# Performance work log

Measured on AMD Instinct MI355X. Metric: run time of the kernel, lower is better.

Reference implementation:

```python
import jax, jax.numpy as jnp
import numpy as np

EPS = 1e-5  # torch BatchNorm1d default

def _silu(x):
    return x * jax.nn.sigmoid(x)

def _bn(x, g, b, rm, rv, axis):
    # eval-mode batchnorm along given channel axis
    shape = [1] * x.ndim
    shape[axis] = -1
    return (x - rm.reshape(shape)) * (g.reshape(shape) / jnp.sqrt(rv.reshape(shape) + EPS)) + b.reshape(shape)

def setup_inputs() -> dict:
    key = jax.random.key(0)
    ks = jax.random.split(key, 12)
    b, n, p, d, r = 64, 256, 12, 128, 2
    x = jax.random.normal(ks[0], (b, n, p, d), dtype=jnp.float32)
    # k branch: Conv1d(p -> 1, k=1, bias=False) + BN(1)
    wk = jax.random.normal(ks[1], (p,), dtype=jnp.float32) / np.sqrt(p)
    bn_k_g = jax.random.uniform(ks[2], (1,), dtype=jnp.float32, minval=0.5, maxval=1.5)
    bn_k_b = 0.1 * jax.random.normal(ks[3], (1,), dtype=jnp.float32)
    bn_k_rm = jnp.zeros((1,), jnp.float32)
    bn_k_rv = jnp.ones((1,), jnp.float32)
    # v branch: Conv1d(d -> d, k=1, bias=False) + BN(d)
    wv = jax.random.normal(ks[4], (d, d), dtype=jnp.float32) / np.sqrt(d)
    bn_v_g = jax.random.uniform(ks[5], (d,), dtype=jnp.float32, minval=0.5, maxval=1.5)
    bn_v_b = 0.1 * jax.random.normal(ks[6], (d,), dtype=jnp.float32)
    bn_v_rm = jnp.zeros((d,), jnp.float32)
    bn_v_rv = jnp.ones((d,), jnp.float32)
    # fc_avg / fc_max: Linear(n, n//r, bias=False) -> GELU -> Linear(n//r, n, bias=False)
    w_avg1 = jax.random.normal(ks[7], (n // r, n), dtype=jnp.float32) / np.sqrt(n)
    w_avg2 = jax.random.normal(ks[8], (n, n // r), dtype=jnp.float32) / np.sqrt(n // r)
    w_max1 = jax.random.normal(ks[9], (n // r, n), dtype=jnp.float32) / np.sqrt(n)
    w_max2 = jax.random.normal(ks[10], (n, n // r), dtype=jnp.float32) / np.sqrt(n // r)
    return dict(x=x, wk=wk, bn_k_g=bn_k_g, bn_k_b=bn_k_b, bn_k_rm=bn_k_rm, bn_k_rv=bn_k_rv,
                wv=wv, bn_v_g=bn_v_g, bn_v_b=bn_v_b, bn_v_rm=bn_v_rm, bn_v_rv=bn_v_rv,
                w_avg1=w_avg1, w_avg2=w_avg2, w_max1=w_max1, w_max2=w_max2)

def _forward(x, wk, bn_k_g, bn_k_b, bn_k_rm, bn_k_rv, wv, bn_v_g, bn_v_b, bn_v_rm, bn_v_rv,
             w_avg1, w_avg2, w_max1, w_max2):
    b, n, p, d = x.shape
    xf = x.reshape(b * n, p, d)
    # squeeze-excite gates: pool over d, FC over n
    avg = jnp.mean(xf, axis=-1).reshape(b, n, p).transpose(0, 2, 1)  # [b,p,n]
    mx = jnp.max(xf, axis=-1).reshape(b, n, p).transpose(0, 2, 1)    # [b,p,n]
    gelu = lambda t: jax.nn.gelu(t, approximate=False)
    avg_g = jax.nn.sigmoid(gelu(avg @ w_avg1.T) @ w_avg2.T).transpose(0, 2, 1)  # [b,n,p]
    max_g = jax.nn.sigmoid(gelu(mx @ w_max1.T) @ w_max2.T).transpose(0, 2, 1)   # [b,n,p]
    # k: 1x1 conv over p channels -> [bn, d], BN(1ch), SiLU, softmax over d
    k_raw = jnp.einsum('bpd,p->bd', xf, wk)
    k = jax.nn.softmax(_silu(k_raw * (bn_k_g / jnp.sqrt(bn_k_rv + EPS)) - bn_k_rm * (bn_k_g / jnp.sqrt(bn_k_rv + EPS)) + bn_k_b), axis=-1)  # [bn,d]
    # v: 1x1 conv over d channels on [bn,d,p], BN(d), SiLU -> [bn,p,d]
    v_raw = jnp.einsum('bpd,ed->bpe', xf, wv)  # channel axis is last here
    v = _silu(_bn(v_raw, bn_v_g, bn_v_b, bn_v_rm, bn_v_rv, axis=2))  # [bn,p,d]
    # y = v @ k : [bn,p];  y_pool = (max+avg) @ v : [bn,d]
    y = jnp.einsum('bpd,bd->bp', v, k)
    pool = (max_g + avg_g).reshape(b * n, p)
    y_pool = jnp.einsum('bp,bpd->bd', pool, v)
    out = y_pool[:, None, :] * y[:, :, None]  # [bn,p,d]
    return out.reshape(b, n, p, d)

def reference(x, wk, bn_k_g, bn_k_b, bn_k_rm, bn_k_rv, wv, bn_v_g, bn_v_b, bn_v_rm, bn_v_rv,
              w_avg1, w_avg2, w_max1, w_max2):
    return _forward(x, wk, bn_k_g, bn_k_b, bn_k_rm, bn_k_rv, wv, bn_v_g, bn_v_b, bn_v_rm, bn_v_rv,
                    w_avg1, w_avg2, w_max1, w_max2)
```

## Files before the change

kernel.cpp:

```cpp
#include <hip/hip_runtime.h>
#include <hip/hip_bf16.h>

#define B_   64
#define N_   256
#define P_   12
#define D_   128
#define BN_  (B_*N_)
#define EPSV 1e-5f

typedef float  f32x4  __attribute__((ext_vector_type(4)));
typedef __bf16 bf16x8 __attribute__((ext_vector_type(8)));
typedef __bf16 bf16x4 __attribute__((ext_vector_type(4)));

__device__ float g_avg[768*256];
__device__ float g_mx [768*256];
__device__ float g_h1 [1536*128];
__device__ float g_pool[BN_*P_];

__device__ inline float sigm_(float x) { return 1.0f / (1.0f + __expf(-x)); }

__device__ inline float dot4_(float4 a, float4 b, float acc) {
  acc = fmaf(a.x, b.x, acc); acc = fmaf(a.y, b.y, acc);
  acc = fmaf(a.z, b.z, acc); acc = fmaf(a.w, b.w, acc);
  return acc;
}

__global__ __launch_bounds__(256) void k1_pool(const float* __restrict__ x) {
  int w = threadIdx.x >> 6, l = threadIdx.x & 63;
  int bn = blockIdx.x * 4 + w;
  const float* xp = x + (size_t)bn * (P_ * D_);
  int half = l >> 5, lane32 = l & 31;
  float s6[6], m6[6];
#pragma unroll
  for (int pp = 0; pp < 6; ++pp) {
    int p = pp * 2 + half;
    float4 v = *(const float4*)(xp + p * D_ + lane32 * 4);
    float s = (v.x + v.y) + (v.z + v.w);
    float m = fmaxf(fmaxf(v.x, v.y), fmaxf(v.z, v.w));
#pragma unroll
    for (int off = 16; off; off >>= 1) {
      s += __shfl_xor(s, off);
      m = fmaxf(m, __shfl_xor(m, off));
    }
    s6[pp] = s * (1.0f / D_);
    m6[pp] = m;
  }
  if (lane32 == 0) {
    int b = bn >> 8, n = bn & 255;
#pragma unroll
    for (int pp = 0; pp < 6; ++pp) {
      int p = pp * 2 + half;
      g_avg[(b * P_ + p) * N_ + n] = s6[pp];
      g_mx [(b * P_ + p) * N_ + n] = m6[pp];
    }
  }
}

__global__ __launch_bounds__(256) void k2_l1(const float* __restrict__ w_avg1,
                                             const float* __restrict__ w_max1) {
  __shared__ float in_t[16 * 256];
  __shared__ float w_t[64 * 68];
  int t = threadIdx.x;
  int rblk = blockIdx.x % 96, cblk = blockIdx.x / 96;
  int rr0 = rblk * 16, c0 = cblk * 64;
  bool mxb = (rr0 >= 768);
  int r768 = mxb ? rr0 - 768 : rr0;
  const float* in = (mxb ? g_mx : g_avg) + (size_t)r768 * 256;
  const float* w1 = mxb ? w_max1 : w_avg1;
#pragma unroll
  for (int i = 0; i < 4; ++i) {
    int F = t + i * 256, r = F >> 6, k4 = F & 63;
    *(float4*)(in_t + r * 256 + k4 * 4) = *(const float4*)(in + r * 256 + k4 * 4);
  }
  int c = t & 63, rq = t >> 6;
  float a0 = 0, a1 = 0, a2 = 0, a3 = 0;
  for (int kc = 0; kc < 4; ++kc) {
    __syncthreads();
#pragma unroll
    for (int i = 0; i < 4; ++i) {
      int F = t + i * 256, cr = F >> 4, k4 = F & 15;
      *(float4*)(w_t + cr * 68 + k4 * 4) =
          *(const float4*)(w1 + (size_t)(c0 + cr) * 256 + kc * 64 + k4 * 4);
    }
    __syncthreads();
#pragma unroll
    for (int k4 = 0; k4 < 16; ++k4) {
      float4 wv4 = *(float4*)(w_t + c * 68 + k4 * 4);
      a0 = dot4_(*(float4*)(in_t + (rq * 4 + 0) * 256 + kc * 64 + k4 * 4), wv4, a0);
      a1 = dot4_(*(float4*)(in_t + (rq * 4 + 1) * 256 + kc * 64 + k4 * 4), wv4, a1);
      a2 = dot4_(*(float4*)(in_t + (rq * 4 + 2) * 256 + kc * 64 + k4 * 4), wv4, a2);
      a3 = dot4_(*(float4*)(in_t + (rq * 4 + 3) * 256 + kc * 64 + k4 * 4), wv4, a3);
    }
  }
  float accs[4] = {a0, a1, a2, a3};
#pragma unroll
  for (int r = 0; r < 4; ++r) {
    float a = accs[r];
    float g = 0.5f * a * (1.0f + erff(a * 0.70710678f));
    g_h1[(size_t)(rr0 + rq * 4 + r) * 128 + c0 + c] = g;
  }
}

__global__ __launch_bounds__(256) void k2_l2(const float* __restrict__ w_avg2,
                                             const float* __restrict__ w_max2) {
  __shared__ float ina_t[16 * 128];
  __shared__ float inm_t[16 * 128];
  __shared__ float wa_t[64 * 68];
  __shared__ float wm_t[64 * 68];
  int t = threadIdx.x;
  int rblk = blockIdx.x % 48, cblk = blockIdx.x / 48;
  int rr0 = rblk * 16, n0 = cblk * 64;
#pragma unroll
  for (int i = 0; i < 2; ++i) {
    int F = t + i * 256, r = F >> 5, k4 = F & 31;
    *(float4*)(ina_t + r * 128 + k4 * 4) = *(const float4*)(g_h1 + (size_t)(rr0 + r) * 128 + k4 * 4);
    *(float4*)(inm_t + r * 128 + k4 * 4) = *(const float4*)(g_h1 + (size_t)(768 + rr0 + r) * 128 + k4 * 4);
  }
  int c = t & 63, rq = t >> 6;
  float aa0=0, aa1=0, aa2=0, aa3=0, am0=0, am1=0, am2=0, am3=0;
  for (int kc = 0; kc < 2; ++kc) {
    __syncthreads();
#pragma unroll
    for (int i = 0; i < 4; ++i) {
      int F = t + i * 256, cr = F >> 4, k4 = F & 15;
      *(float4*)(wa_t + cr * 68 + k4 * 4) =
          *(const float4*)(w_avg2 + (size_t)(n0 + cr) * 128 + kc * 64 + k4 * 4);
      *(float4*)(wm_t + cr * 68 + k4 * 4) =
          *(const float4*)(w_max2 + (size_t)(n0 + cr) * 128 + kc * 64 + k4 * 4);
    }
    __syncthreads();
#pragma unroll
    for (int k4 = 0; k4 < 16; ++k4) {
      float4 wa4 = *(float4*)(wa_t + c * 68 + k4 * 4);
      float4 wm4 = *(float4*)(wm_t + c * 68 + k4 * 4);
      float4 i0 = *(float4*)(ina_t + (rq * 4 + 0) * 128 + kc * 64 + k4 * 4);
      float4 i1 = *(float4*)(ina_t + (rq * 4 + 1) * 128 + kc * 64 + k4 * 4);
      float4 i2 = *(float4*)(ina_t + (rq * 4 + 2) * 128 + kc * 64 + k4 * 4);
      float4 i3 = *(float4*)(ina_t + (rq * 4 + 3) * 128 + kc * 64 + k4 * 4);
      aa0 = dot4_(i0, wa4, aa0); aa1 = dot4_(i1, wa4, aa1);
      aa2 = dot4_(i2, wa4, aa2); aa3 = dot4_(i3, wa4, aa3);
      float4 j0 = *(float4*)(inm_t + (rq * 4 + 0) * 128 + kc * 64 + k4 * 4);
      float4 j1 = *(float4*)(inm_t + (rq * 4 + 1) * 128 + kc * 64 + k4 * 4);
      float4 j2 = *(float4*)(inm_t + (rq * 4 + 2) * 128 + kc * 64 + k4 * 4);
      float4 j3 = *(float4*)(inm_t + (rq * 4 + 3) * 128 + kc * 64 + k4 * 4);
      am0 = dot4_(j0, wm4, am0); am1 = dot4_(j1, wm4, am1);
      am2 = dot4_(j2, wm4, am2); am3 = dot4_(j3, wm4, am3);
    }
  }
  float va[4] = {aa0, aa1, aa2, aa3};
  float vm[4] = {am0, am1, am2, am3};
#pragma unroll
  for (int r = 0; r < 4; ++r) {
    int rr = rr0 + rq * 4 + r;
    int b = rr / 12, p = rr % 12;
    float pv = sigm_(va[r]) + sigm_(vm[r]);
    g_pool[((size_t)b * 256 + (n0 + c)) * 12 + p] = pv;
  }
}

__global__ __launch_bounds__(256) void k3_main(
    const float* __restrict__ x,  const float* __restrict__ wk,
    const float* __restrict__ kg, const float* __restrict__ kb,
    const float* __restrict__ krm, const float* __restrict__ krv,
    const float* __restrict__ wv,
    const float* __restrict__ vg, const float* __restrict__ vb,
    const float* __restrict__ vrm, const float* __restrict__ vrv,
    float* __restrict__ out) {
  __shared__ __align__(16) __bf16 wv_lds[128 * 128];
  __shared__ float sv_l[128], tv_l[128];
  __shared__ float k_lds[4][128];
  __shared__ float yp_l[4][128];
  __shared__ __align__(16) float y_l[4][16];

  int t = threadIdx.x, w = t >> 6, l = t & 63;
  if (t < 128) {
    float s = vg[t] * rsqrtf(vrv[t] + EPSV);
    sv_l[t] = s;
    tv_l[t] = vb[t] - vrm[t] * s;
  }
  __syncthreads();
  {
    int e = t >> 1, dh = (t & 1) * 64;
    float s = sv_l[e];
    int swz = (e & 7) << 4;
#pragma unroll
    for (int i = 0; i < 16; ++i) {
      float4 v4 = *(const float4*)(wv + (size_t)e * 128 + dh + i * 4);
      bf16x4 h;
      h[0] = (__bf16)(v4.x * s); h[1] = (__bf16)(v4.y * s);
      h[2] = (__bf16)(v4.z * s); h[3] = (__bf16)(v4.w * s);
      int byte = (e * 256 + (dh + i * 4) * 2) ^ swz;
      *(bf16x4*)((char*)wv_lds + byte) = h;
    }
  }
  float ksc = kg[0] * rsqrtf(krv[0] + EPSV);
  float kbs = kb[0] - krm[0] * ksc;
  float wkl[P_];
#pragma unroll
  for (int p = 0; p < P_; ++p) wkl[p] = wk[p];
  __syncthreads();

  int arow = (l & 15) > 11 ? 11 : (l & 15);
  int ak = (l >> 4) * 8;
  int bcol = l & 15;
  int bko = (l >> 4) * 16;
  int p0 = (l >> 4) * 4;
  bool rows_ok = (p0 < 12);

  float tv_e[8];
#pragma unroll
  for (int nt = 0; nt < 8; ++nt) tv_e[nt] = tv_l[bcol + nt * 16];

  for (int it = 0; it < 4; ++it) {
    int bn = blockIdx.x * 16 + it * 4 + w;
    const float* xp = x + (size_t)bn * (P_ * D_);

    float pool_r[4] = {0.f, 0.f, 0.f, 0.f};
    if (rows_ok) {
      const float* pp = g_pool + (size_t)bn * 12 + p0;
#pragma unroll
      for (int r = 0; r < 4; ++r) pool_r[r] = pp[r];
    }

    bf16x8 afr[4];
#pragma unroll
    for (int ks = 0; ks < 4; ++ks) {
      const float* src = xp + arow * 128 + ks * 32 + ak;
      float4 lo = *(const float4*)(src);
      float4 hi = *(const float4*)(src + 4);
      bf16x8 a;
      a[0] = (__bf16)lo.x; a[1] = (__bf16)lo.y; a[2] = (__bf16)lo.z; a[3] = (__bf16)lo.w;
      a[4] = (__bf16)hi.x; a[5] = (__bf16)hi.y; a[6] = (__bf16)hi.z; a[7] = (__bf16)hi.w;
      afr[ks] = a;
    }

    float kr0 = 0, kr1 = 0;
#pragma unroll
    for (int p = 0; p < P_; ++p) {
      float2 xv = *(const float2*)(xp + p * 128 + 2 * l);
      kr0 = fmaf(xv.x, wkl[p], kr0);
      kr1 = fmaf(xv.y, wkl[p], kr1);
    }
    float z0 = kr0 * ksc + kbs, z1 = kr1 * ksc + kbs;
    z0 = z0 * sigm_(z0);
    z1 = z1 * sigm_(z1);
    float mmax = fmaxf(z0, z1);
#pragma unroll
    for (int off = 32; off; off >>= 1) mmax = fmaxf(mmax, __shfl_xor(mmax, off));
    float e0 = __expf(z0 - mmax), e1 = __expf(z1 - mmax);
    float es = e0 + e1;
#pragma unroll
    for (int off = 32; off; off >>= 1) es += __shfl_xor(es, off);
    float inv = 1.0f / es;

    float2 kw; kw.x = e0 * inv; kw.y = e1 * inv;
    *(float2*)(&k_lds[w][2 * l]) = kw;
    float k_e[8];
#pragma unroll
    for (int nt = 0; nt < 8; ++nt) k_e[nt] = k_lds[w][bcol + nt * 16];

    f32x4 acc[8];
#pragma unroll
    for (int nt = 0; nt < 8; ++nt) acc[nt] = (f32x4){0.f, 0.f, 0.f, 0.f};
#pragma unroll
    for (int nt = 0; nt < 8; ++nt) {
      int er = bcol + nt * 16;
      int base = er * 256;
      int sw = (er & 7) << 4;
#pragma unroll
      for (int ks = 0; ks < 4; ++ks) {
        int byte = (base + ks * 64 + bko) ^ sw;
        bf16x8 bfr = *(const bf16x8*)((const char*)wv_lds + byte);
        acc[nt] = __builtin_amdgcn_mfma_f32_16x16x32_bf16(afr[ks], bfr, acc[nt], 0, 0, 0);
      }
    }

    float y_r[4] = {0.f, 0.f, 0.f, 0.f};
    float ypp[8];
#pragma unroll
    for (int nt = 0; nt < 8; ++nt) {
      float s = 0.f;
#pragma unroll
      for (int r = 0; r < 4; ++r) {
        float a = acc[nt][r] + tv_e[nt];
        float v = a * sigm_(a);
        y_r[r] = fmaf(v, k_e[nt], y_r[r]);
        s = fmaf(pool_r[r], v, s);
      }
      ypp[nt] = s;
    }
#pragma unroll
    for (int r = 0; r < 4; ++r) {
#pragma unroll
      for (int off = 8; off; off >>= 1) y_r[r] += __shfl_xor(y_r[r], off);
    }
#pragma unroll
    for (int nt = 0; nt < 8; ++nt) {
      ypp[nt] += __shfl_xor(ypp[nt], 16);
      ypp[nt] += __shfl_xor(ypp[nt], 32);
    }

    if (bcol == 0 && rows_ok) {
      float4 yq; yq.x = y_r[0]; yq.y = y_r[1]; yq.z = y_r[2]; yq.w = y_r[3];
      *(float4*)(&y_l[w][p0]) = yq;
    }
    if (l < 16) {
#pragma unroll
      for (int nt = 0; nt < 8; ++nt) yp_l[w][bcol + nt * 16] = ypp[nt];
    }
    float2 yp2 = *(const float2*)(&yp_l[w][2 * l]);
    float yv[P_];
#pragma unroll
    for (int p = 0; p < P_; ++p) yv[p] = y_l[w][p];

    float* op = out + (size_t)bn * (P_ * D_);
#pragma unroll
    for (int p = 0; p < P_; ++p) {
      float2 o;
      o.x = yv[p] * yp2.x;
      o.y = yv[p] * yp2.y;
      *(float2*)(op + p * 128 + 2 * l) = o;
    }
  }
}

extern "C" void kernel_launch(void* const* d_in, const int* in_sizes, int n_in,
                              void* d_out, int out_size, void* d_ws, size_t ws_size,
                              hipStream_t stream) {
  const float* x   = (const float*)d_in[0];
  const float* wk  = (const float*)d_in[1];
  const float* kg  = (const float*)d_in[2];
  const float* kbb = (const float*)d_in[3];
  const float* krm = (const float*)d_in[4];
  const float* krv = (const float*)d_in[5];
  const float* wvp = (const float*)d_in[6];
  const float* vg  = (const float*)d_in[7];
  const float* vbb = (const float*)d_in[8];
  const float* vrm = (const float*)d_in[9];
  const float* vrv = (const float*)d_in[10];
  const float* wa1 = (const float*)d_in[11];
  const float* wa2 = (const float*)d_in[12];
  const float* wm1 = (const float*)d_in[13];
  const float* wm2 = (const float*)d_in[14];
  float* out = (float*)d_out;

  k1_pool<<<4096, 256, 0, stream>>>(x);
  k2_l1<<<192, 256, 0, stream>>>(wa1, wm1);
  k2_l2<<<192, 256, 0, stream>>>(wa2, wm2);
  k3_main<<<1024, 256, 0, stream>>>(x, wk, kg, kbb, krm, krv, wvp, vg, vbb, vrm, vrv, out);
}
```

Before: 114.5 us.

## Move k-softmax and bf16 conversion of x into the pooling kernel

The pooling kernel now also computes the k-branch conv, BN, SiLU and softmax, and writes x converted to bf16 into a global scratch buffer. The main kernel reads precomputed k and the bf16 x instead of re-reading fp32 x twice, and its grid doubles to 2048 blocks with two rows per wave. The intent is to cut main-kernel global reads and per-iteration compute in half. The cost is an extra 25 MB bf16 write plus a k buffer write and read, and the main kernel's per-block wv LDS setup is amortized over fewer rows.

Result: slower. 129.4 us (+13.0%).

```diff
diff --git a/kernel.cpp b/kernel.cpp
--- a/kernel.cpp
+++ b/kernel.cpp
@@ -12,10 +12,12 @@
 typedef __bf16 bf16x8 __attribute__((ext_vector_type(8)));
 typedef __bf16 bf16x4 __attribute__((ext_vector_type(4)));
 
-__device__ float g_avg[768*256];
-__device__ float g_mx [768*256];
-__device__ float g_h1 [1536*128];
-__device__ float g_pool[BN_*P_];
+__device__ float  g_avg[768*256];
+__device__ float  g_mx [768*256];
+__device__ float  g_h1 [1536*128];
+__device__ float  g_pool[BN_*P_];
+__device__ float  g_k  [BN_*D_];
+__device__ __bf16 g_xbf[(size_t)BN_*P_*D_];
 
 __device__ inline float sigm_(float x) { return 1.0f / (1.0f + __expf(-x)); }
 
@@ -25,16 +27,31 @@
   return acc;
 }
 
-__global__ __launch_bounds__(256) void k1_pool(const float* __restrict__ x) {
+__global__ __launch_bounds__(256) void k1_pool(const float* __restrict__ x,
+                                               const float* __restrict__ wk,
+                                               const float* __restrict__ kg,
+                                               const float* __restrict__ kb,
+                                               const float* __restrict__ krm,
+                                               const float* __restrict__ krv) {
   int w = threadIdx.x >> 6, l = threadIdx.x & 63;
   int bn = blockIdx.x * 4 + w;
   const float* xp = x + (size_t)bn * (P_ * D_);
+  __bf16* xbp = g_xbf + (size_t)bn * (P_ * D_);
   int half = l >> 5, lane32 = l & 31;
+  float ksc = kg[0] * rsqrtf(krv[0] + EPSV);
+  float kbs = kb[0] - krm[0] * ksc;
   float s6[6], m6[6];
+  float kr0 = 0, kr1 = 0, kr2 = 0, kr3 = 0;
 #pragma unroll
   for (int pp = 0; pp < 6; ++pp) {
     int p = pp * 2 + half;
     float4 v = *(const float4*)(xp + p * D_ + lane32 * 4);
+    bf16x4 h;
+    h[0] = (__bf16)v.x; h[1] = (__bf16)v.y; h[2] = (__bf16)v.z; h[3] = (__bf16)v.w;
+    *(bf16x4*)(xbp + p * D_ + lane32 * 4) = h;
+    float wkp = wk[p];
+    kr0 = fmaf(v.x, wkp, kr0); kr1 = fmaf(v.y, wkp, kr1);
+    kr2 = fmaf(v.z, wkp, kr2); kr3 = fmaf(v.w, wkp, kr3);
     float s = (v.x + v.y) + (v.z + v.w);
     float m = fmaxf(fmaxf(v.x, v.y), fmaxf(v.z, v.w));
 #pragma unroll
@@ -44,6 +61,25 @@
     }
     s6[pp] = s * (1.0f / D_);
     m6[pp] = m;
+  }
+  kr0 += __shfl_xor(kr0, 32); kr1 += __shfl_xor(kr1, 32);
+  kr2 += __shfl_xor(kr2, 32); kr3 += __shfl_xor(kr3, 32);
+  float z0 = kr0 * ksc + kbs, z1 = kr1 * ksc + kbs;
+  float z2 = kr2 * ksc + kbs, z3 = kr3 * ksc + kbs;
+  z0 = z0 * sigm_(z0); z1 = z1 * sigm_(z1);
+  z2 = z2 * sigm_(z2); z3 = z3 * sigm_(z3);
+  float mx = fmaxf(fmaxf(z0, z1), fmaxf(z2, z3));
+#pragma unroll
+  for (int off = 16; off; off >>= 1) mx = fmaxf(mx, __shfl_xor(mx, off));
+  float e0 = __expf(z0 - mx), e1 = __expf(z1 - mx);
+  float e2 = __expf(z2 - mx), e3 = __expf(z3 - mx);
+  float es = (e0 + e1) + (e2 + e3);
+#pragma unroll
+  for (int off = 16; off; off >>= 1) es += __shfl_xor(es, off);
+  float inv = 1.0f / es;
+  if (half == 0) {
+    float4 kk; kk.x = e0 * inv; kk.y = e1 * inv; kk.z = e2 * inv; kk.w = e3 * inv;
+    *(float4*)(g_k + (size_t)bn * D_ + lane32 * 4) = kk;
   }
   if (lane32 == 0) {
     int b = bn >> 8, n = bn & 255;
@@ -159,16 +195,12 @@
 }
 
 __global__ __launch_bounds__(256) void k3_main(
-    const float* __restrict__ x,  const float* __restrict__ wk,
-    const float* __restrict__ kg, const float* __restrict__ kb,
-    const float* __restrict__ krm, const float* __restrict__ krv,
     const float* __restrict__ wv,
     const float* __restrict__ vg, const float* __restrict__ vb,
     const float* __restrict__ vrm, const float* __restrict__ vrv,
     float* __restrict__ out) {
   __shared__ __align__(16) __bf16 wv_lds[128 * 128];
   __shared__ float sv_l[128], tv_l[128];
-  __shared__ float k_lds[4][128];
   __shared__ float yp_l[4][128];
   __shared__ __align__(16) float y_l[4][16];
 
@@ -193,11 +225,6 @@
       *(bf16x4*)((char*)wv_lds + byte) = h;
     }
   }
-  float ksc = kg[0] * rsqrtf(krv[0] + EPSV);
-  float kbs = kb[0] - krm[0] * ksc;
-  float wkl[P_];
-#pragma unroll
-  for (int p = 0; p < P_; ++p) wkl[p] = wk[p];
   __syncthreads();
 
   int arow = (l & 15) > 11 ? 11 : (l & 15);
@@ -211,9 +238,8 @@
 #pragma unroll
   for (int nt = 0; nt < 8; ++nt) tv_e[nt] = tv_l[bcol + nt * 16];
 
-  for (int it = 0; it < 4; ++it) {
-    int bn = blockIdx.x * 16 + it * 4 + w;
-    const float* xp = x + (size_t)bn * (P_ * D_);
+  for (int it = 0; it < 2; ++it) {
+    int bn = blockIdx.x * 8 + it * 4 + w;
 
     float pool_r[4] = {0.f, 0.f, 0.f, 0.f};
     if (rows_ok) {
@@ -222,42 +248,16 @@
       for (int r = 0; r < 4; ++r) pool_r[r] = pp[r];
     }
 
+    const float* kp = g_k + (size_t)bn * D_;
+    float k_e[8];
+#pragma unroll
+    for (int nt = 0; nt < 8; ++nt) k_e[nt] = kp[bcol + nt * 16];
+
+    const __bf16* xbp = g_xbf + (size_t)bn * (P_ * D_) + arow * D_;
     bf16x8 afr[4];
 #pragma unroll
-    for (int ks = 0; ks < 4; ++ks) {
-      const float* src = xp + arow * 128 + ks * 32 + ak;
-      float4 lo = *(const float4*)(src);
-      float4 hi = *(const float4*)(src + 4);
-      bf16x8 a;
-      a[0] = (__bf16)lo.x; a[1] = (__bf16)lo.y; a[2] = (__bf16)lo.z; a[3] = (__bf16)lo.w;
-      a[4] = (__bf16)hi.x; a[5] = (__bf16)hi.y; a[6] = (__bf16)hi.z; a[7] = (__bf16)hi.w;
-      afr[ks] = a;
-    }
-
-    float kr0 = 0, kr1 = 0;
-#pragma unroll
-    for (int p = 0; p < P_; ++p) {
-      float2 xv = *(const float2*)(xp + p * 128 + 2 * l);
-      kr0 = fmaf(xv.x, wkl[p], kr0);
-      kr1 = fmaf(xv.y, wkl[p], kr1);
-    }
-    float z0 = kr0 * ksc + kbs, z1 = kr1 * ksc + kbs;
-    z0 = z0 * sigm_(z0);
-    z1 = z1 * sigm_(z1);
-    float mmax = fmaxf(z0, z1);
-#pragma unroll
-    for (int off = 32; off; off >>= 1) mmax = fmaxf(mmax, __shfl_xor(mmax, off));
-    float e0 = __expf(z0 - mmax), e1 = __expf(z1 - mmax);
-    float es = e0 + e1;
-#pragma unroll
-    for (int off = 32; off; off >>= 1) es += __shfl_xor(es, off);
-    float inv = 1.0f / es;
-
-    float2 kw; kw.x = e0 * inv; kw.y = e1 * inv;
-    *(float2*)(&k_lds[w][2 * l]) = kw;
-    float k_e[8];
-#pragma unroll
-    for (int nt = 0; nt < 8; ++nt) k_e[nt] = k_lds[w][bcol + nt * 16];
+    for (int ks = 0; ks < 4; ++ks)
+      afr[ks] = *(const bf16x8*)(xbp + ks * 32 + ak);
 
     f32x4 acc[8];
 #pragma unroll
@@ -344,8 +344,8 @@
   const float* wm2 = (const float*)d_in[14];
   float* out = (float*)d_out;
 
-  k1_pool<<<4096, 256, 0, stream>>>(x);
+  k1_pool<<<4096, 256, 0, stream>>>(x, wk, kg, kbb, krm, krv);
   k2_l1<<<192, 256, 0, stream>>>(wa1, wm1);
   k2_l2<<<192, 256, 0, stream>>>(wa2, wm2);
-  k3_main<<<1024, 256, 0, stream>>>(x, wk, kg, kbb, krm, krv, wvp, vg, vbb, vrm, vrv, out);
-}
+  k3_main<<<2048, 256, 0, stream>>>(wvp, vg, vbb, vrm, vrv, out);
+}
```
